# Kernel tuning notes

Hardware: AMD Instinct MI355X
Metric: run time of the kernel (lower is better)

The kernel has to match this reference:

```python
import jax, jax.numpy as jnp
import numpy as np

N_NODES = 100000
N_EDGES = 1600000
N_FEATS = 128
N_CLASSES = 40
K_HOPS = 3


def setup_inputs() -> dict:
    key = jax.random.key(0)
    k1, k2, k3, k4 = jax.random.split(key, 4)
    x = jax.random.normal(k1, (N_NODES, N_FEATS), dtype=jnp.float32)
    edge_index = jax.random.randint(k2, (2, N_EDGES), 0, N_NODES, dtype=jnp.int64)
    edge_weight = jax.random.uniform(k3, (N_EDGES,), dtype=jnp.float32)
    # Linear layer of SGConv (bias=False): [num_feats, num_classes]
    W = jax.random.normal(k4, (N_FEATS, N_CLASSES), dtype=jnp.float32) / np.sqrt(N_FEATS)
    return {"x": x, "edge_index": edge_index, "edge_weight": edge_weight, "W": W}


def reference(x, edge_index, edge_weight, W):
    # SGConv forward: gcn_norm (symmetric, no self-loops), K hops of
    # edge-weighted gather/scatter aggregation, then linear (lin_first=False).
    row, col = edge_index[0], edge_index[1]
    # symmetric normalization: deg from target-node scatter of edge weights
    deg = jax.ops.segment_sum(edge_weight, col, num_segments=N_NODES)
    deg_inv_sqrt = jnp.where(deg > 0, jax.lax.rsqrt(jnp.maximum(deg, 1e-30)), 0.0)
    norm = deg_inv_sqrt[row] * edge_weight * deg_inv_sqrt[col]  # [E]
    h = x
    for _ in range(K_HOPS):
        msgs = h[row] * norm[:, None]                 # [E, F] gather + scale
        h = jax.ops.segment_sum(msgs, col, num_segments=N_NODES)  # [N, F] scatter-add
    return h @ W  # [N, num_classes]
```

## Files before the change

kernel.cpp:

```cpp
#include <hip/hip_runtime.h>
#include <hip/hip_fp16.h>

namespace {
constexpr int NN = 100000;
constexpr int NE = 1600000;
constexpr int NF = 128;
constexpr int NC = 40;
constexpr int HP = 64;
constexpr int NB = (NN + 255) / 256;
constexpr int EPB = 4096;
constexpr int EBK = (NE + EPB - 1) / EPB;
constexpr int CAP = 6144;
constexpr float FIX = 1048576.0f;
constexpr int NPB = 51;
constexpr int HB  = (NN + NPB - 1) / NPB;
constexpr int TS  = 2048;
}

struct alignas(16) H8 { __half2 a, b, c, d; };

__device__ inline __half2 f2h2(float x, float y) {
    return __halves2half2(__float2half_rn(x), __float2half_rn(y));
}

__global__ __launch_bounds__(256) void k_bucket(const int* __restrict__ col,
                                                const int* __restrict__ row,
                                                const float* __restrict__ w,
                                                unsigned int* __restrict__ cursor,
                                                int2* __restrict__ bstage) {
    __shared__ unsigned int lhist[NB];
    __shared__ unsigned int lbase[NB];
    __shared__ unsigned int lrank[NB];
    int t = threadIdx.x;
    for (int i = t; i < NB; i += 256) { lhist[i] = 0u; lrank[i] = 0u; }
    __syncthreads();
    int e0 = blockIdx.x * EPB;
    int e1 = min(e0 + EPB, NE);
    for (int e = e0 + t; e < e1; e += 256)
        atomicAdd(&lhist[col[e] >> 8], 1u);
    __syncthreads();
    for (int i = t; i < NB; i += 256) {
        unsigned c = lhist[i];
        lbase[i] = c ? atomicAdd(&cursor[i], c) : 0u;
    }
    __syncthreads();
    for (int e = e0 + t; e < e1; e += 256) {
        int c = col[e];
        int b = c >> 8;
        unsigned r = atomicAdd(&lrank[b], 1u);
        int2 v;
        v.x = (row[e] & 0x1FFFF) | ((c & 255) << 17);
        v.y = __float_as_int(w[e]);
        bstage[(size_t)b * CAP + lbase[b] + r] = v;
    }
}

__global__ __launch_bounds__(512) void k_bscan(const unsigned int* __restrict__ cursor,
                                               int* __restrict__ bbase,
                                               int* __restrict__ offs) {
    __shared__ int s[512];
    int t = threadIdx.x;
    int v = (t < NB) ? (int)cursor[t] : 0;
    s[t] = v;
    __syncthreads();
    for (int off = 1; off < 512; off <<= 1) {
        int add = (t >= off) ? s[t - off] : 0;
        __syncthreads();
        s[t] += add;
        __syncthreads();
    }
    if (t < NB) bbase[t] = s[t] - v;
    if (t == NB) bbase[NB] = s[NB - 1];
    if (t == 0)  offs[NN] = NE;
}

__global__ __launch_bounds__(256) void k_sortgemm(const int2* __restrict__ bstage,
                                                  const int* __restrict__ bbase,
                                                  const float* __restrict__ x,
                                                  const float* __restrict__ W,
                                                  int* __restrict__ offs,
                                                  float* __restrict__ invdis,
                                                  int2* __restrict__ pair,
                                                  __half* __restrict__ z0) {
    __shared__ unsigned long long lpk[256];
    __shared__ int ls[256];
    __shared__ float ldis[256];
    __shared__ unsigned int lrank[256];
    __shared__ float4 lW[NF * NC / 4];
    int t = threadIdx.x;
    int b = blockIdx.x;
    int base = bbase[b];
    int cnt  = bbase[b + 1] - base;
    {
        const float4* Wg = (const float4*)W;
#pragma unroll
        for (int i = 0; i < 5; ++i) lW[t + i * 256] = Wg[t + i * 256];
    }
    lpk[t] = 0ull;
    lrank[t] = 0u;
    __syncthreads();
    const int2* bs = bstage + (size_t)b * CAP;
    for (int j = t; j < cnt; j += 256) {
        int2 s = bs[j];
        int cl = (s.x >> 17) & 255;
        unsigned long long q =
            (unsigned long long)(unsigned)(__int_as_float(s.y) * FIX + 0.5f);
        atomicAdd(&lpk[cl], (1ull << 40) | q);
    }
    __syncthreads();
    int myc = (int)(lpk[t] >> 40);
    float deg = (float)(lpk[t] & ((1ull << 40) - 1)) * (1.0f / FIX);
    float dis = (deg > 0.f) ? rsqrtf(deg) : 0.f;
    ldis[t] = dis;
    ls[t] = myc;
    __syncthreads();
    for (int off = 1; off < 256; off <<= 1) {
        int add = (t >= off) ? ls[t - off] : 0;
        __syncthreads();
        ls[t] += add;
        __syncthreads();
    }
    int start = ls[t] - myc;
    int n = b * 256 + t;
    if (n < NN) {
        offs[n] = base + start;
        invdis[n] = sqrtf(fmaxf(deg, 0.f));
    }
    ls[t] = start;
    __syncthreads();
    for (int j = t; j < cnt; j += 256) {
        int2 s = bs[j];
        int cl = (s.x >> 17) & 255;
        unsigned r = atomicAdd(&lrank[cl], 1u);
        float d = ldis[cl];
        int2 v;
        v.x = s.x & 0x1FFFF;
        v.y = __float_as_int(__int_as_float(s.y) * d * d);
        pair[base + ls[cl] + r] = v;
    }
    if (n < NN) {
        const float4* xr = (const float4*)(x + (size_t)n * NF);
        float acc[NC];
#pragma unroll
        for (int j = 0; j < NC; ++j) acc[j] = 0.f;
        for (int k4 = 0; k4 < NF / 4; ++k4) {
            float4 xv = xr[k4];
#pragma unroll
            for (int kk = 0; kk < 4; ++kk) {
                float xk = (kk == 0) ? xv.x : (kk == 1) ? xv.y : (kk == 2) ? xv.z : xv.w;
                int k = k4 * 4 + kk;
#pragma unroll
                for (int j4 = 0; j4 < 10; ++j4) {
                    float4 wv = lW[k * 10 + j4];
                    acc[j4 * 4 + 0] += xk * wv.x;
                    acc[j4 * 4 + 1] += xk * wv.y;
                    acc[j4 * 4 + 2] += xk * wv.z;
                    acc[j4 * 4 + 3] += xk * wv.w;
                }
            }
        }
        float sc = ldis[t];
        H8* o = (H8*)(z0 + (size_t)n * HP);
#pragma unroll
        for (int g = 0; g < 5; ++g) {
            H8 v;
            v.a = f2h2(acc[g * 8 + 0] * sc, acc[g * 8 + 1] * sc);
            v.b = f2h2(acc[g * 8 + 2] * sc, acc[g * 8 + 3] * sc);
            v.c = f2h2(acc[g * 8 + 4] * sc, acc[g * 8 + 5] * sc);
            v.d = f2h2(acc[g * 8 + 6] * sc, acc[g * 8 + 7] * sc);
            o[g] = v;
        }
    }
}

template <bool FINAL>
__global__ __launch_bounds__(256) void k_hop(const int* __restrict__ offs,
                                             const int2* __restrict__ pair,
                                             const __half* __restrict__ hin,
                                             __half* __restrict__ houth,
                                             float* __restrict__ houtf,
                                             const float* __restrict__ invdis) {
    __shared__ int2 tile[TS];
    __shared__ int erange[2];
    int t = threadIdx.x;
    int g = t / 5;
    int n = blockIdx.x * NPB + g;
    bool active = (t < NPB * 5) && (n < NN);
    int vo = (t - g * 5) * 8;
    int s0 = 0, s1 = 0;
    if (active) {
        s0 = offs[n];
        s1 = offs[n + 1];
    }
    if (t == 0) {
        int n0 = blockIdx.x * NPB;
        int nl = min(n0 + NPB, NN);
        erange[0] = offs[n0];
        erange[1] = offs[nl];
    }
    __syncthreads();
    int E0 = erange[0], E1 = erange[1];
    float acc[8];
#pragma unroll
    for (int j = 0; j < 8; ++j) acc[j] = 0.f;
    int i = s0;
#define ACC8(m, wgt) { float2 f_;                                        \
    f_ = __half22float2((m).a); acc[0] += f_.x * (wgt); acc[1] += f_.y * (wgt); \
    f_ = __half22float2((m).b); acc[2] += f_.x * (wgt); acc[3] += f_.y * (wgt); \
    f_ = __half22float2((m).c); acc[4] += f_.x * (wgt); acc[5] += f_.y * (wgt); \
    f_ = __half22float2((m).d); acc[6] += f_.x * (wgt); acc[7] += f_.y * (wgt); }
    for (int t0 = E0; t0 < E1; t0 += TS) {
        int lim = min(t0 + TS, E1);
        int cnt = lim - t0;
        for (int j = t; j < cnt; j += 256) tile[j] = pair[t0 + j];
        __syncthreads();
        if (active) {
            int hi = min(s1, lim);
            for (; i + 4 <= hi; i += 4) {
                int2 p0 = tile[i - t0];
                int2 p1 = tile[i + 1 - t0];
                int2 p2 = tile[i + 2 - t0];
                int2 p3 = tile[i + 3 - t0];
                H8 m0 = *(const H8*)(hin + (size_t)p0.x * HP + vo);
                H8 m1 = *(const H8*)(hin + (size_t)p1.x * HP + vo);
                H8 m2 = *(const H8*)(hin + (size_t)p2.x * HP + vo);
                H8 m3 = *(const H8*)(hin + (size_t)p3.x * HP + vo);
                float w0 = __int_as_float(p0.y);
                float w1 = __int_as_float(p1.y);
                float w2 = __int_as_float(p2.y);
                float w3 = __int_as_float(p3.y);
                ACC8(m0, w0) ACC8(m1, w1) ACC8(m2, w2) ACC8(m3, w3)
            }
            for (; i < hi; ++i) {
                int2 p0 = tile[i - t0];
                H8 m0 = *(const H8*)(hin + (size_t)p0.x * HP + vo);
                float w0 = __int_as_float(p0.y);
                ACC8(m0, w0)
            }
        }
        __syncthreads();
    }
#undef ACC8
    if (active) {
        if (FINAL) {
            float sc = invdis[n];
            float* o = houtf + (size_t)n * NC + vo;
            float4 v0 = {acc[0] * sc, acc[1] * sc, acc[2] * sc, acc[3] * sc};
            float4 v1 = {acc[4] * sc, acc[5] * sc, acc[6] * sc, acc[7] * sc};
            *(float4*)(o) = v0;
            *(float4*)(o + 4) = v1;
        } else {
            H8 v;
            v.a = f2h2(acc[0], acc[1]);
            v.b = f2h2(acc[2], acc[3]);
            v.c = f2h2(acc[4], acc[5]);
            v.d = f2h2(acc[6], acc[7]);
            *(H8*)(houth + (size_t)n * HP + vo) = v;
        }
    }
}

extern "C" void kernel_launch(void* const* d_in, const int* in_sizes, int n_in,
                              void* d_out, int out_size, void* d_ws, size_t ws_size,
                              hipStream_t stream) {
    const float* x  = (const float*)d_in[0];
    const int*   ei = (const int*)d_in[1];
    const float* w  = (const float*)d_in[2];
    const float* W  = (const float*)d_in[3];
    const int* row = ei;
    const int* col = ei + NE;
    float* out = (float*)d_out;

    char* base = (char*)d_ws;
    int2* bstage = (int2*)base;
    __half* hb   = (__half*)base;
    char* p = base + (size_t)NB * CAP * 8;
    __half* ha = (__half*)p;        p += (size_t)NN * HP * 2;
    int2* pair = (int2*)p;          p += (size_t)NE * 8;
    int*  offs = (int*)p;           p += (size_t)(NN + 1) * 4;
    int*  bbase = (int*)p;          p += (size_t)(NB + 1) * 4;
    float* invdis = (float*)p;      p += (size_t)NN * 4;
    unsigned int* cursor = (unsigned int*)p;

    hipMemsetAsync(cursor, 0, (size_t)NB * 4, stream);
    k_bucket<<<EBK, 256, 0, stream>>>(col, row, w, cursor, bstage);
    k_bscan<<<1, 512, 0, stream>>>(cursor, bbase, offs);
    k_sortgemm<<<NB, 256, 0, stream>>>(bstage, bbase, x, W, offs, invdis, pair, ha);

    k_hop<false><<<HB, 256, 0, stream>>>(offs, pair, ha, hb, nullptr, nullptr);
    k_hop<false><<<HB, 256, 0, stream>>>(offs, pair, hb, ha, nullptr, nullptr);
    k_hop<true ><<<HB, 256, 0, stream>>>(offs, pair, ha, nullptr, out, invdis);
}
```

Measured before the change: 264.2 us.

## Run x@W GEMM alongside edge bucketing and defer dis scaling to first hop

The dense x@W projection moves out of the sort kernel into a fused launch, where it runs in separate blocks concurrently with the edge bucketing pass. Because deg_inv_sqrt is not yet known at that point, the sort kernel writes each node's dis into padding slot 40 of the fp16 row, and the first hop multiplies each edge weight by the source row's stored dis. This takes the GEMM off the critical path after the bucket scan and shortens the sort kernel. The cost is an extra 4-byte gather per edge in the first hop and the unscaled GEMM output being rounded to fp16 before scaling.

Result: no change. 267.3 us (+1.2%).

```diff
diff --git a/kernel.cpp b/kernel.cpp
--- a/kernel.cpp
+++ b/kernel.cpp
@@ -23,35 +23,81 @@
     return __halves2half2(__float2half_rn(x), __float2half_rn(y));
 }
 
-__global__ __launch_bounds__(256) void k_bucket(const int* __restrict__ col,
-                                                const int* __restrict__ row,
-                                                const float* __restrict__ w,
-                                                unsigned int* __restrict__ cursor,
-                                                int2* __restrict__ bstage) {
-    __shared__ unsigned int lhist[NB];
-    __shared__ unsigned int lbase[NB];
-    __shared__ unsigned int lrank[NB];
+__global__ __launch_bounds__(256) void k_fused(const int* __restrict__ col,
+                                               const int* __restrict__ row,
+                                               const float* __restrict__ w,
+                                               unsigned int* __restrict__ cursor,
+                                               int2* __restrict__ bstage,
+                                               const float* __restrict__ x,
+                                               const float* __restrict__ W,
+                                               __half* __restrict__ g0) {
+    __shared__ char sb[20480];
     int t = threadIdx.x;
-    for (int i = t; i < NB; i += 256) { lhist[i] = 0u; lrank[i] = 0u; }
-    __syncthreads();
-    int e0 = blockIdx.x * EPB;
-    int e1 = min(e0 + EPB, NE);
-    for (int e = e0 + t; e < e1; e += 256)
-        atomicAdd(&lhist[col[e] >> 8], 1u);
-    __syncthreads();
-    for (int i = t; i < NB; i += 256) {
-        unsigned c = lhist[i];
-        lbase[i] = c ? atomicAdd(&cursor[i], c) : 0u;
-    }
-    __syncthreads();
-    for (int e = e0 + t; e < e1; e += 256) {
-        int c = col[e];
-        int b = c >> 8;
-        unsigned r = atomicAdd(&lrank[b], 1u);
-        int2 v;
-        v.x = (row[e] & 0x1FFFF) | ((c & 255) << 17);
-        v.y = __float_as_int(w[e]);
-        bstage[(size_t)b * CAP + lbase[b] + r] = v;
+    if (blockIdx.x < (unsigned)EBK) {
+        unsigned int* lhist = (unsigned int*)sb;
+        unsigned int* lbase = lhist + NB;
+        unsigned int* lrank = lbase + NB;
+        for (int i = t; i < NB; i += 256) { lhist[i] = 0u; lrank[i] = 0u; }
+        __syncthreads();
+        int e0 = blockIdx.x * EPB;
+        int e1 = min(e0 + EPB, NE);
+        for (int e = e0 + t; e < e1; e += 256)
+            atomicAdd(&lhist[col[e] >> 8], 1u);
+        __syncthreads();
+        for (int i = t; i < NB; i += 256) {
+            unsigned c = lhist[i];
+            lbase[i] = c ? atomicAdd(&cursor[i], c) : 0u;
+        }
+        __syncthreads();
+        for (int e = e0 + t; e < e1; e += 256) {
+            int c = col[e];
+            int b = c >> 8;
+            unsigned r = atomicAdd(&lrank[b], 1u);
+            int2 v;
+            v.x = (row[e] & 0x1FFFF) | ((c & 255) << 17);
+            v.y = __float_as_int(w[e]);
+            bstage[(size_t)b * CAP + lbase[b] + r] = v;
+        }
+    } else {
+        float4* lW = (float4*)sb;
+        {
+            const float4* Wg = (const float4*)W;
+#pragma unroll
+            for (int i = 0; i < 5; ++i) lW[t + i * 256] = Wg[t + i * 256];
+        }
+        __syncthreads();
+        int n = (blockIdx.x - EBK) * 256 + t;
+        if (n >= NN) return;
+        const float4* xr = (const float4*)(x + (size_t)n * NF);
+        float acc[NC];
+#pragma unroll
+        for (int j = 0; j < NC; ++j) acc[j] = 0.f;
+        for (int k4 = 0; k4 < NF / 4; ++k4) {
+            float4 xv = xr[k4];
+#pragma unroll
+            for (int kk = 0; kk < 4; ++kk) {
+                float xk = (kk == 0) ? xv.x : (kk == 1) ? xv.y : (kk == 2) ? xv.z : xv.w;
+                int k = k4 * 4 + kk;
+#pragma unroll
+                for (int j4 = 0; j4 < 10; ++j4) {
+                    float4 wv = lW[k * 10 + j4];
+                    acc[j4 * 4 + 0] += xk * wv.x;
+                    acc[j4 * 4 + 1] += xk * wv.y;
+                    acc[j4 * 4 + 2] += xk * wv.z;
+                    acc[j4 * 4 + 3] += xk * wv.w;
+                }
+            }
+        }
+        H8* o = (H8*)(g0 + (size_t)n * HP);
+#pragma unroll
+        for (int g = 0; g < 5; ++g) {
+            H8 v;
+            v.a = f2h2(acc[g * 8 + 0], acc[g * 8 + 1]);
+            v.b = f2h2(acc[g * 8 + 2], acc[g * 8 + 3]);
+            v.c = f2h2(acc[g * 8 + 4], acc[g * 8 + 5]);
+            v.d = f2h2(acc[g * 8 + 6], acc[g * 8 + 7]);
+            o[g] = v;
+        }
     }
 }
 
@@ -74,28 +120,20 @@
     if (t == 0)  offs[NN] = NE;
 }
 
-__global__ __launch_bounds__(256) void k_sortgemm(const int2* __restrict__ bstage,
-                                                  const int* __restrict__ bbase,
-                                                  const float* __restrict__ x,
-                                                  const float* __restrict__ W,
-                                                  int* __restrict__ offs,
-                                                  float* __restrict__ invdis,
-                                                  int2* __restrict__ pair,
-                                                  __half* __restrict__ z0) {
+__global__ __launch_bounds__(256) void k_sort(const int2* __restrict__ bstage,
+                                              const int* __restrict__ bbase,
+                                              int* __restrict__ offs,
+                                              float* __restrict__ invdis,
+                                              int2* __restrict__ pair,
+                                              __half* __restrict__ g0) {
     __shared__ unsigned long long lpk[256];
     __shared__ int ls[256];
     __shared__ float ldis[256];
     __shared__ unsigned int lrank[256];
-    __shared__ float4 lW[NF * NC / 4];
     int t = threadIdx.x;
     int b = blockIdx.x;
     int base = bbase[b];
     int cnt  = bbase[b + 1] - base;
-    {
-        const float4* Wg = (const float4*)W;
-#pragma unroll
-        for (int i = 0; i < 5; ++i) lW[t + i * 256] = Wg[t + i * 256];
-    }
     lpk[t] = 0ull;
     lrank[t] = 0u;
     __syncthreads();
@@ -125,6 +163,7 @@
     if (n < NN) {
         offs[n] = base + start;
         invdis[n] = sqrtf(fmaxf(deg, 0.f));
+        *(float*)(g0 + (size_t)n * HP + 40) = dis;
     }
     ls[t] = start;
     __syncthreads();
@@ -138,42 +177,9 @@
         v.y = __float_as_int(__int_as_float(s.y) * d * d);
         pair[base + ls[cl] + r] = v;
     }
-    if (n < NN) {
-        const float4* xr = (const float4*)(x + (size_t)n * NF);
-        float acc[NC];
-#pragma unroll
-        for (int j = 0; j < NC; ++j) acc[j] = 0.f;
-        for (int k4 = 0; k4 < NF / 4; ++k4) {
-            float4 xv = xr[k4];
-#pragma unroll
-            for (int kk = 0; kk < 4; ++kk) {
-                float xk = (kk == 0) ? xv.x : (kk == 1) ? xv.y : (kk == 2) ? xv.z : xv.w;
-                int k = k4 * 4 + kk;
-#pragma unroll
-                for (int j4 = 0; j4 < 10; ++j4) {
-                    float4 wv = lW[k * 10 + j4];
-                    acc[j4 * 4 + 0] += xk * wv.x;
-                    acc[j4 * 4 + 1] += xk * wv.y;
-                    acc[j4 * 4 + 2] += xk * wv.z;
-                    acc[j4 * 4 + 3] += xk * wv.w;
-                }
-            }
-        }
-        float sc = ldis[t];
-        H8* o = (H8*)(z0 + (size_t)n * HP);
-#pragma unroll
-        for (int g = 0; g < 5; ++g) {
-            H8 v;
-            v.a = f2h2(acc[g * 8 + 0] * sc, acc[g * 8 + 1] * sc);
-            v.b = f2h2(acc[g * 8 + 2] * sc, acc[g * 8 + 3] * sc);
-            v.c = f2h2(acc[g * 8 + 4] * sc, acc[g * 8 + 5] * sc);
-            v.d = f2h2(acc[g * 8 + 6] * sc, acc[g * 8 + 7] * sc);
-            o[g] = v;
-        }
-    }
-}
-
-template <bool FINAL>
+}
+
+template <bool FINAL, bool WD>
 __global__ __launch_bounds__(256) void k_hop(const int* __restrict__ offs,
                                              const int2* __restrict__ pair,
                                              const __half* __restrict__ hin,
@@ -221,20 +227,32 @@
                 int2 p1 = tile[i + 1 - t0];
                 int2 p2 = tile[i + 2 - t0];
                 int2 p3 = tile[i + 3 - t0];
-                H8 m0 = *(const H8*)(hin + (size_t)p0.x * HP + vo);
-                H8 m1 = *(const H8*)(hin + (size_t)p1.x * HP + vo);
-                H8 m2 = *(const H8*)(hin + (size_t)p2.x * HP + vo);
-                H8 m3 = *(const H8*)(hin + (size_t)p3.x * HP + vo);
+                const __half* r0 = hin + (size_t)p0.x * HP;
+                const __half* r1 = hin + (size_t)p1.x * HP;
+                const __half* r2 = hin + (size_t)p2.x * HP;
+                const __half* r3 = hin + (size_t)p3.x * HP;
+                H8 m0 = *(const H8*)(r0 + vo);
+                H8 m1 = *(const H8*)(r1 + vo);
+                H8 m2 = *(const H8*)(r2 + vo);
+                H8 m3 = *(const H8*)(r3 + vo);
                 float w0 = __int_as_float(p0.y);
                 float w1 = __int_as_float(p1.y);
                 float w2 = __int_as_float(p2.y);
                 float w3 = __int_as_float(p3.y);
+                if (WD) {
+                    w0 *= *(const float*)(r0 + 40);
+                    w1 *= *(const float*)(r1 + 40);
+                    w2 *= *(const float*)(r2 + 40);
+                    w3 *= *(const float*)(r3 + 40);
+                }
                 ACC8(m0, w0) ACC8(m1, w1) ACC8(m2, w2) ACC8(m3, w3)
             }
             for (; i < hi; ++i) {
                 int2 p0 = tile[i - t0];
-                H8 m0 = *(const H8*)(hin + (size_t)p0.x * HP + vo);
+                const __half* r0 = hin + (size_t)p0.x * HP;
+                H8 m0 = *(const H8*)(r0 + vo);
                 float w0 = __int_as_float(p0.y);
+                if (WD) w0 *= *(const float*)(r0 + 40);
                 ACC8(m0, w0)
             }
         }
@@ -283,11 +301,11 @@
     unsigned int* cursor = (unsigned int*)p;
 
     hipMemsetAsync(cursor, 0, (size_t)NB * 4, stream);
-    k_bucket<<<EBK, 256, 0, stream>>>(col, row, w, cursor, bstage);
+    k_fused<<<EBK + NB, 256, 0, stream>>>(col, row, w, cursor, bstage, x, W, ha);
     k_bscan<<<1, 512, 0, stream>>>(cursor, bbase, offs);
-    k_sortgemm<<<NB, 256, 0, stream>>>(bstage, bbase, x, W, offs, invdis, pair, ha);
-
-    k_hop<false><<<HB, 256, 0, stream>>>(offs, pair, ha, hb, nullptr, nullptr);
-    k_hop<false><<<HB, 256, 0, stream>>>(offs, pair, hb, ha, nullptr, nullptr);
-    k_hop<true ><<<HB, 256, 0, stream>>>(offs, pair, ha, nullptr, out, invdis);
-}
+    k_sort<<<NB, 256, 0, stream>>>(bstage, bbase, offs, invdis, pair, ha);
+
+    k_hop<false, true ><<<HB, 256, 0, stream>>>(offs, pair, ha, hb, nullptr, nullptr);
+    k_hop<false, false><<<HB, 256, 0, stream>>>(offs, pair, hb, ha, nullptr, nullptr);
+    k_hop<true,  false><<<HB, 256, 0, stream>>>(offs, pair, ha, nullptr, out, invdis);
+}
```

## Split fused sort+GEMM kernel into separate sort and GEMM kernels

Applied to the files above, without the earlier changes.

The combined bucket-sort plus projection kernel is split into a 512-thread sort kernel and a standalone 256-thread GEMM kernel, passing the per-node inverse-sqrt degree through a new global buffer. The sort now stages bucket records in shared memory using nontemporal loads and records each edge's rank from the degree atomic's return value. This removes the second global read of the staging buffer and the second atomic pass. The split lets each kernel use its own occupancy and launch shape, at the cost of an extra launch, ~50KB of shared memory per sort block, and a small extra global round-trip for the scale factors.

Result: slower. 271.3 us (+2.7%).

```diff
diff --git a/kernel.cpp b/kernel.cpp
--- a/kernel.cpp
+++ b/kernel.cpp
@@ -74,102 +74,116 @@
     if (t == 0)  offs[NN] = NE;
 }
 
-__global__ __launch_bounds__(256) void k_sortgemm(const int2* __restrict__ bstage,
-                                                  const int* __restrict__ bbase,
-                                                  const float* __restrict__ x,
-                                                  const float* __restrict__ W,
-                                                  int* __restrict__ offs,
-                                                  float* __restrict__ invdis,
-                                                  int2* __restrict__ pair,
-                                                  __half* __restrict__ z0) {
+__global__ __launch_bounds__(512) void k_sort(const int2* __restrict__ bstage,
+                                              const int* __restrict__ bbase,
+                                              int* __restrict__ offs,
+                                              float* __restrict__ invdis,
+                                              float* __restrict__ dis_g,
+                                              int2* __restrict__ pair) {
+    __shared__ int2 rec[CAP];
+    __shared__ unsigned char rk8[CAP];
     __shared__ unsigned long long lpk[256];
     __shared__ int ls[256];
     __shared__ float ldis[256];
-    __shared__ unsigned int lrank[256];
-    __shared__ float4 lW[NF * NC / 4];
     int t = threadIdx.x;
     int b = blockIdx.x;
     int base = bbase[b];
     int cnt  = bbase[b + 1] - base;
-    {
-        const float4* Wg = (const float4*)W;
-#pragma unroll
-        for (int i = 0; i < 5; ++i) lW[t + i * 256] = Wg[t + i * 256];
-    }
-    lpk[t] = 0ull;
-    lrank[t] = 0u;
-    __syncthreads();
-    const int2* bs = bstage + (size_t)b * CAP;
-    for (int j = t; j < cnt; j += 256) {
-        int2 s = bs[j];
+    if (t < 256) lpk[t] = 0ull;
+    __syncthreads();
+    const unsigned long long* bs64 = (const unsigned long long*)(bstage + (size_t)b * CAP);
+    for (int j = t; j < cnt; j += 512) {
+        unsigned long long u = __builtin_nontemporal_load(bs64 + j);
+        int2 s; s.x = (int)(unsigned)u; s.y = (int)(u >> 32);
+        rec[j] = s;
         int cl = (s.x >> 17) & 255;
         unsigned long long q =
             (unsigned long long)(unsigned)(__int_as_float(s.y) * FIX + 0.5f);
-        atomicAdd(&lpk[cl], (1ull << 40) | q);
-    }
-    __syncthreads();
-    int myc = (int)(lpk[t] >> 40);
-    float deg = (float)(lpk[t] & ((1ull << 40) - 1)) * (1.0f / FIX);
-    float dis = (deg > 0.f) ? rsqrtf(deg) : 0.f;
-    ldis[t] = dis;
-    ls[t] = myc;
+        unsigned long long old = atomicAdd(&lpk[cl], (1ull << 40) | q);
+        rk8[j] = (unsigned char)(old >> 40);
+    }
+    __syncthreads();
+    if (t < 256) {
+        int myc = (int)(lpk[t] >> 40);
+        float deg = (float)(lpk[t] & ((1ull << 40) - 1)) * (1.0f / FIX);
+        float dis = (deg > 0.f) ? rsqrtf(deg) : 0.f;
+        ldis[t] = dis;
+        ls[t] = myc;
+        int n = b * 256 + t;
+        if (n < NN) {
+            invdis[n] = sqrtf(fmaxf(deg, 0.f));
+            dis_g[n]  = dis;
+        }
+    }
     __syncthreads();
     for (int off = 1; off < 256; off <<= 1) {
-        int add = (t >= off) ? ls[t - off] : 0;
-        __syncthreads();
-        ls[t] += add;
-        __syncthreads();
-    }
-    int start = ls[t] - myc;
-    int n = b * 256 + t;
-    if (n < NN) {
-        offs[n] = base + start;
-        invdis[n] = sqrtf(fmaxf(deg, 0.f));
-    }
-    ls[t] = start;
-    __syncthreads();
-    for (int j = t; j < cnt; j += 256) {
-        int2 s = bs[j];
+        int add = (t < 256 && t >= off) ? ls[t - off] : 0;
+        __syncthreads();
+        if (t < 256) ls[t] += add;
+        __syncthreads();
+    }
+    if (t < 256) {
+        int myc = (int)(lpk[t] >> 40);
+        ls[t] -= myc;
+        int n = b * 256 + t;
+        if (n < NN) offs[n] = base + ls[t];
+    }
+    __syncthreads();
+    for (int j = t; j < cnt; j += 512) {
+        int2 s = rec[j];
         int cl = (s.x >> 17) & 255;
-        unsigned r = atomicAdd(&lrank[cl], 1u);
         float d = ldis[cl];
         int2 v;
         v.x = s.x & 0x1FFFF;
         v.y = __float_as_int(__int_as_float(s.y) * d * d);
-        pair[base + ls[cl] + r] = v;
-    }
-    if (n < NN) {
-        const float4* xr = (const float4*)(x + (size_t)n * NF);
-        float acc[NC];
-#pragma unroll
-        for (int j = 0; j < NC; ++j) acc[j] = 0.f;
-        for (int k4 = 0; k4 < NF / 4; ++k4) {
-            float4 xv = xr[k4];
-#pragma unroll
-            for (int kk = 0; kk < 4; ++kk) {
-                float xk = (kk == 0) ? xv.x : (kk == 1) ? xv.y : (kk == 2) ? xv.z : xv.w;
-                int k = k4 * 4 + kk;
-#pragma unroll
-                for (int j4 = 0; j4 < 10; ++j4) {
-                    float4 wv = lW[k * 10 + j4];
-                    acc[j4 * 4 + 0] += xk * wv.x;
-                    acc[j4 * 4 + 1] += xk * wv.y;
-                    acc[j4 * 4 + 2] += xk * wv.z;
-                    acc[j4 * 4 + 3] += xk * wv.w;
-                }
+        pair[base + ls[cl] + rk8[j]] = v;
+    }
+}
+
+__global__ __launch_bounds__(256) void k_gemm(const float* __restrict__ x,
+                                              const float* __restrict__ W,
+                                              const float* __restrict__ dis_g,
+                                              __half* __restrict__ z0) {
+    __shared__ float4 lW[NF * NC / 4];
+    int t = threadIdx.x;
+    {
+        const float4* Wg = (const float4*)W;
+#pragma unroll
+        for (int i = 0; i < 5; ++i) lW[t + i * 256] = Wg[t + i * 256];
+    }
+    __syncthreads();
+    int n = blockIdx.x * 256 + t;
+    if (n >= NN) return;
+    const float4* xr = (const float4*)(x + (size_t)n * NF);
+    float acc[NC];
+#pragma unroll
+    for (int j = 0; j < NC; ++j) acc[j] = 0.f;
+    for (int k4 = 0; k4 < NF / 4; ++k4) {
+        float4 xv = xr[k4];
+#pragma unroll
+        for (int kk = 0; kk < 4; ++kk) {
+            float xk = (kk == 0) ? xv.x : (kk == 1) ? xv.y : (kk == 2) ? xv.z : xv.w;
+            int k = k4 * 4 + kk;
+#pragma unroll
+            for (int j4 = 0; j4 < 10; ++j4) {
+                float4 wv = lW[k * 10 + j4];
+                acc[j4 * 4 + 0] += xk * wv.x;
+                acc[j4 * 4 + 1] += xk * wv.y;
+                acc[j4 * 4 + 2] += xk * wv.z;
+                acc[j4 * 4 + 3] += xk * wv.w;
             }
         }
-        float sc = ldis[t];
-        H8* o = (H8*)(z0 + (size_t)n * HP);
-#pragma unroll
-        for (int g = 0; g < 5; ++g) {
-            H8 v;
-            v.a = f2h2(acc[g * 8 + 0] * sc, acc[g * 8 + 1] * sc);
-            v.b = f2h2(acc[g * 8 + 2] * sc, acc[g * 8 + 3] * sc);
-            v.c = f2h2(acc[g * 8 + 4] * sc, acc[g * 8 + 5] * sc);
-            v.d = f2h2(acc[g * 8 + 6] * sc, acc[g * 8 + 7] * sc);
-            o[g] = v;
-        }
+    }
+    float sc = dis_g[n];
+    H8* o = (H8*)(z0 + (size_t)n * HP);
+#pragma unroll
+    for (int g = 0; g < 5; ++g) {
+        H8 v;
+        v.a = f2h2(acc[g * 8 + 0] * sc, acc[g * 8 + 1] * sc);
+        v.b = f2h2(acc[g * 8 + 2] * sc, acc[g * 8 + 3] * sc);
+        v.c = f2h2(acc[g * 8 + 4] * sc, acc[g * 8 + 5] * sc);
+        v.d = f2h2(acc[g * 8 + 6] * sc, acc[g * 8 + 7] * sc);
+        o[g] = v;
     }
 }
 
@@ -280,12 +294,14 @@
     int*  offs = (int*)p;           p += (size_t)(NN + 1) * 4;
     int*  bbase = (int*)p;          p += (size_t)(NB + 1) * 4;
     float* invdis = (float*)p;      p += (size_t)NN * 4;
+    float* dis_g = (float*)p;       p += (size_t)NN * 4;
     unsigned int* cursor = (unsigned int*)p;
 
     hipMemsetAsync(cursor, 0, (size_t)NB * 4, stream);
     k_bucket<<<EBK, 256, 0, stream>>>(col, row, w, cursor, bstage);
     k_bscan<<<1, 512, 0, stream>>>(cursor, bbase, offs);
-    k_sortgemm<<<NB, 256, 0, stream>>>(bstage, bbase, x, W, offs, invdis, pair, ha);
+    k_sort<<<NB, 512, 0, stream>>>(bstage, bbase, offs, invdis, dis_g, pair);
+    k_gemm<<<NB, 256, 0, stream>>>(x, W, dis_g, ha);
 
     k_hop<false><<<HB, 256, 0, stream>>>(offs, pair, ha, hb, nullptr, nullptr);
     k_hop<false><<<HB, 256, 0, stream>>>(offs, pair, hb, ha, nullptr, nullptr);
```
